# Performance work log

Hardware: AMD Instinct MI355X
Metric: run time of the kernel (lower is better)

## Reference

```python
import jax, jax.numpy as jnp
import numpy as np

B, T, I, H, O = 64, 512, 256, 512, 256

def setup_inputs() -> dict:
    key = jax.random.key(0)
    ks = jax.random.split(key, 12)
    s = 1.0 / np.sqrt(H)
    u = lambda k, shp: jax.random.uniform(k, shp, jnp.float32, -s, s)
    return {
        'x': jax.random.normal(ks[0], (B, T, I), jnp.float32),
        'w_ih0': u(ks[1], (H, I)),  'w_hh0': u(ks[2], (H, H)),
        'b_ih0': u(ks[3], (H,)),    'b_hh0': u(ks[4], (H,)),
        'w_ih1': u(ks[5], (H, H)),  'w_hh1': u(ks[6], (H, H)),
        'b_ih1': u(ks[7], (H,)),    'b_hh1': u(ks[8], (H,)),
        'fc_w': u(ks[9], (O, H)),   'fc_b': u(ks[10], (O,)),
    }

def _rnn_layer(inp, w_ih, w_hh, b_ih, b_hh):
    # inp: [B, T, F] -> precompute input projection once (one big GEMM)
    xp = jnp.einsum('btf,hf->bth', inp, w_ih) + b_ih + b_hh  # [B, T, H]
    def step(h, xt):
        h = jnp.tanh(xt + h @ w_hh.T)  # [B, H]
        return h, h
    h0 = jnp.zeros((inp.shape[0], w_hh.shape[0]), inp.dtype)
    hT, outs = jax.lax.scan(step, h0, jnp.swapaxes(xp, 0, 1))  # outs: [T, B, H]
    return jnp.swapaxes(outs, 0, 1), hT

def reference(x, w_ih0, w_hh0, b_ih0, b_hh0, w_ih1, w_hh1, b_ih1, b_hh1, fc_w, fc_b):
    out0, h0f = _rnn_layer(x, w_ih0, w_hh0, b_ih0, b_hh0)
    out1, h1f = _rnn_layer(out0, w_ih1, w_hh1, b_ih1, b_hh1)
    hidden = jnp.stack([h0f, h1f])                  # [n_layers, B, H]
    out = out1.reshape(-1, out1.shape[-1]) @ fc_w.T + fc_b  # [B*T, O]
    return out, hidden
```

## Files before the change

kernel.cpp:

```cpp
#include <hip/hip_runtime.h>

#define B_  64
#define T_  512
#define I_  256
#define H_  512
#define O_  256
#define JW  2
#define BS  16
#define NG  (B_ / BS)
#define FLAG_STRIDE 32

typedef __attribute__((ext_vector_type(8))) __bf16 bf16x8;
typedef __attribute__((ext_vector_type(4))) float f32x4;

__device__ __forceinline__ unsigned short f2bf(float f) {
    unsigned int u = __float_as_uint(f);
    unsigned int r = (u + 0x7fffu + ((u >> 16) & 1u)) >> 16;
    return (unsigned short)r;
}

__device__ __forceinline__ float tanh_fast(float x) {
    float e = __expf(2.0f * x);
    float d = e + 1.0f;
    float r;
    asm("v_rcp_f32 %0, %1" : "=v"(r) : "v"(d));
    return 1.0f - 2.0f * r;
}

__global__ void cvt_kernel(const float* __restrict__ in, unsigned short* __restrict__ out, int n4) {
    int i = blockIdx.x * blockDim.x + threadIdx.x;
    if (i >= n4) return;
    float4 f = reinterpret_cast<const float4*>(in)[i];
    ushort4 o;
    o.x = f2bf(f.x); o.y = f2bf(f.y); o.z = f2bf(f.z); o.w = f2bf(f.w);
    reinterpret_cast<ushort4*>(out)[i] = o;
}

__global__ __launch_bounds__(256) void gemm_kernel(
    const unsigned short* __restrict__ A,
    const unsigned short* __restrict__ Bw,
    const float* __restrict__ b0,
    const float* __restrict__ b1,
    float* __restrict__ C,
    int M, int N, int K)
{
    const int m0 = blockIdx.x * 64;
    const int n0 = blockIdx.y * 64;
    const int tid = threadIdx.x;
    const int wv = tid >> 6;
    const int l = tid & 63;
    const int lr = l & 15;
    const int lk = (l >> 4) * 8;
    const int arow = m0 + wv * 16 + lr;

    f32x4 acc[4] = {{0,0,0,0},{0,0,0,0},{0,0,0,0},{0,0,0,0}};
    const int nks = K / 32;
    for (int ks = 0; ks < nks; ++ks) {
        bf16x8 a = *reinterpret_cast<const bf16x8*>(A + (size_t)arow * K + ks * 32 + lk);
        #pragma unroll
        for (int nt = 0; nt < 4; ++nt) {
            bf16x8 b = *reinterpret_cast<const bf16x8*>(Bw + (size_t)(n0 + nt * 16 + lr) * K + ks * 32 + lk);
            acc[nt] = __builtin_amdgcn_mfma_f32_16x16x32_bf16(a, b, acc[nt], 0, 0, 0);
        }
    }
    #pragma unroll
    for (int nt = 0; nt < 4; ++nt) {
        #pragma unroll
        for (int r = 0; r < 4; ++r) {
            int row = m0 + wv * 16 + (l >> 4) * 4 + r;
            int col = n0 + nt * 16 + lr;
            float v = acc[nt][r];
            if (b0) v += b0[col];
            if (b1) v += b1[col];
            C[(size_t)row * N + col] = v;
        }
    }
}

#define LDW8(ARR, BASE) \
    asm volatile( \
        "global_load_dwordx4 %0, %8, %9 offset:0\n\t" \
        "global_load_dwordx4 %1, %8, %9 offset:64\n\t" \
        "global_load_dwordx4 %2, %8, %9 offset:128\n\t" \
        "global_load_dwordx4 %3, %8, %9 offset:192\n\t" \
        "global_load_dwordx4 %4, %8, %9 offset:256\n\t" \
        "global_load_dwordx4 %5, %8, %9 offset:320\n\t" \
        "global_load_dwordx4 %6, %8, %9 offset:384\n\t" \
        "global_load_dwordx4 %7, %8, %9 offset:448\n\t" \
        "s_waitcnt vmcnt(0)" \
        : "=&v"(ARR[0]), "=&v"(ARR[1]), "=&v"(ARR[2]), "=&v"(ARR[3]), \
          "=&v"(ARR[4]), "=&v"(ARR[5]), "=&v"(ARR[6]), "=&v"(ARR[7]) \
        : "v"(BASE), "s"(w))

#define STORE_BUNDLE(PK, VHP, VOUT) \
    asm volatile( \
        "global_store_dword %16, %0, %21 sc0 sc1\n\t" \
        "global_store_dword %16, %1, %21 offset:1024 sc0 sc1\n\t" \
        "global_store_dword %16, %2, %21 offset:2048 sc0 sc1\n\t" \
        "global_store_dword %16, %3, %21 offset:3072 sc0 sc1\n\t" \
        "global_store_dword %16, %4, %21 offset:32 sc0 sc1\n\t" \
        "global_store_dword %16, %5, %21 offset:1056 sc0 sc1\n\t" \
        "global_store_dword %16, %6, %21 offset:2080 sc0 sc1\n\t" \
        "global_store_dword %16, %7, %21 offset:3104 sc0 sc1\n\t" \
        "global_store_dword %16, %8, %21 offset:64 sc0 sc1\n\t" \
        "global_store_dword %16, %9, %21 offset:1088 sc0 sc1\n\t" \
        "global_store_dword %16, %10, %21 offset:2112 sc0 sc1\n\t" \
        "global_store_dword %16, %11, %21 offset:3136 sc0 sc1\n\t" \
        "global_store_dword %16, %12, %21 offset:96 sc0 sc1\n\t" \
        "global_store_dword %16, %13, %21 offset:1120 sc0 sc1\n\t" \
        "global_store_dword %16, %14, %21 offset:2144 sc0 sc1\n\t" \
        "global_store_dword %16, %15, %21 offset:3168 sc0 sc1\n\t" \
        "global_store_dword %17, %0, %22\n\t" \
        "global_store_dword %18, %1, %22\n\t" \
        "global_store_dword %19, %2, %22\n\t" \
        "global_store_dword %20, %3, %22\n\t" \
        "global_store_dword %17, %4, %22 offset:32\n\t" \
        "global_store_dword %18, %5, %22 offset:32\n\t" \
        "global_store_dword %19, %6, %22 offset:32\n\t" \
        "global_store_dword %20, %7, %22 offset:32\n\t" \
        "global_store_dword %17, %8, %22 offset:64\n\t" \
        "global_store_dword %18, %9, %22 offset:64\n\t" \
        "global_store_dword %19, %10, %22 offset:64\n\t" \
        "global_store_dword %20, %11, %22 offset:64\n\t" \
        "global_store_dword %17, %12, %22 offset:96\n\t" \
        "global_store_dword %18, %13, %22 offset:96\n\t" \
        "global_store_dword %19, %14, %22 offset:96\n\t" \
        "global_store_dword %20, %15, %22 offset:96\n\t" \
        "s_waitcnt vmcnt(16)" \
        :: "v"(PK[0]), "v"(PK[1]), "v"(PK[2]), "v"(PK[3]), \
           "v"(PK[4]), "v"(PK[5]), "v"(PK[6]), "v"(PK[7]), \
           "v"(PK[8]), "v"(PK[9]), "v"(PK[10]), "v"(PK[11]), \
           "v"(PK[12]), "v"(PK[13]), "v"(PK[14]), "v"(PK[15]), \
           "v"(VHP), "v"(VOUT[0]), "v"(VOUT[1]), "v"(VOUT[2]), "v"(VOUT[3]), \
           "s"(h_buf), "s"(out_bf) \
        : "memory")

__global__ __launch_bounds__(256, 1) void recur_kernel(
    const float* __restrict__ xp,
    const unsigned short* __restrict__ w,
    unsigned short* __restrict__ out_bf,
    float* __restrict__ h_final,
    unsigned short* __restrict__ h_buf,
    int* __restrict__ flags)
{
    __shared__ __align__(16) unsigned short lds[16 * 272];

    const int bid = blockIdx.x;
    const int g   = bid >> 1;
    const int jw  = bid & 1;
    const int pjw = jw ^ 1;
    const int b0  = g * BS;
    const int tid = threadIdx.x;
    const int wv  = tid >> 6;
    const int l   = tid & 63;
    const int lr  = l & 15;
    const int lk  = (l >> 4) * 8;
    const int jn0 = jw * 256 + wv * 64;
    const int arow = b0 + lr;
    const int erow_l = (l >> 4) * 4;
    const int erow_g = b0 + erow_l;

    bf16x8 bwo[4][8], bwp[4][8];
    #pragma unroll
    for (int nt = 0; nt < 4; ++nt) {
        unsigned int vo = (unsigned)((jn0 + nt * 16 + lr) * (H_ * 2) + jw  * 512 + lk * 2);
        unsigned int vp = (unsigned)((jn0 + nt * 16 + lr) * (H_ * 2) + pjw * 512 + lk * 2);
        LDW8(bwo[nt], vo);
        LDW8(bwp[nt], vp);
    }

    unsigned int vxpr[4], vout[4];
    #pragma unroll
    for (int r = 0; r < 4; ++r) {
        vxpr[r] = (unsigned)((((erow_g + r) * T_) * H_ + jn0 + lr) * 4);
        vout[r] = (unsigned)(((erow_g + r) * T_) * H_ * 2 + (jn0 + lr) * 2);
    }
    const unsigned int vaf0p = (unsigned)(arow * (H_ * 2) + pjw * 512 + lk * 2);
    const unsigned int vhs0  = (unsigned)(erow_g * (H_ * 2) + (jn0 + lr) * 2);
    const unsigned int fpeer = (unsigned)((bid ^ 1) * FLAG_STRIDE * 4);
    const unsigned int fself = (unsigned)(bid * FLAG_STRIDE * 4);
    const int cb = wv * 32 + (lr >> 1);

    {
        float xpr[16];
        asm volatile(
            "global_load_dword %0, %16, %20\n\t"
            "global_load_dword %1, %17, %20\n\t"
            "global_load_dword %2, %18, %20\n\t"
            "global_load_dword %3, %19, %20\n\t"
            "global_load_dword %4, %16, %20 offset:64\n\t"
            "global_load_dword %5, %17, %20 offset:64\n\t"
            "global_load_dword %6, %18, %20 offset:64\n\t"
            "global_load_dword %7, %19, %20 offset:64\n\t"
            "global_load_dword %8, %16, %20 offset:128\n\t"
            "global_load_dword %9, %17, %20 offset:128\n\t"
            "global_load_dword %10, %18, %20 offset:128\n\t"
            "global_load_dword %11, %19, %20 offset:128\n\t"
            "global_load_dword %12, %16, %20 offset:192\n\t"
            "global_load_dword %13, %17, %20 offset:192\n\t"
            "global_load_dword %14, %18, %20 offset:192\n\t"
            "global_load_dword %15, %19, %20 offset:192\n\t"
            "s_waitcnt vmcnt(0)"
            : "=&v"(xpr[0]), "=&v"(xpr[1]), "=&v"(xpr[2]), "=&v"(xpr[3]),
              "=&v"(xpr[4]), "=&v"(xpr[5]), "=&v"(xpr[6]), "=&v"(xpr[7]),
              "=&v"(xpr[8]), "=&v"(xpr[9]), "=&v"(xpr[10]), "=&v"(xpr[11]),
              "=&v"(xpr[12]), "=&v"(xpr[13]), "=&v"(xpr[14]), "=&v"(xpr[15])
            : "v"(vxpr[0]), "v"(vxpr[1]), "v"(vxpr[2]), "v"(vxpr[3]), "s"(xp));

        unsigned int pk[16];
        #pragma unroll
        for (int nt = 0; nt < 4; ++nt)
            #pragma unroll
            for (int r = 0; r < 4; ++r) {
                int i = nt * 4 + r;
                float hv = tanh_fast(xpr[i]);
                unsigned int mine = f2bf(hv);
                unsigned int oth = (unsigned int)__shfl_xor((int)mine, 1, 64);
                pk[i] = mine | (oth << 16);
            }
        if (!(lr & 1)) {
            unsigned int* lw = (unsigned int*)lds;
            #pragma unroll
            for (int nt = 0; nt < 4; ++nt)
                #pragma unroll
                for (int r = 0; r < 4; ++r)
                    lw[(erow_l + r) * 136 + cb + nt * 8] = pk[nt * 4 + r];
            unsigned int vh_p = vhs0 + (1u << 16);
            STORE_BUNDLE(pk, vh_p, vout);
        }
        __syncthreads();
        if (tid == 0) {
            int nv = 1;
            asm volatile("global_store_dword %0, %1, %2 sc0 sc1"
                         :: "v"(fself), "v"(nv), "s"(flags) : "memory");
        }
        #pragma unroll
        for (int r = 0; r < 4; ++r) { vxpr[r] += H_ * 4; vout[r] += H_ * 2; }
    }

    for (int t = 1; t < T_; ++t) {
        f32x4 acc[4] = {{0,0,0,0},{0,0,0,0},{0,0,0,0},{0,0,0,0}};
        bf16x8 afo[8];
        const unsigned short* lrb = lds + lr * 272 + lk;
        #pragma unroll
        for (int i = 0; i < 8; ++i)
            afo[i] = *reinterpret_cast<const bf16x8*>(lrb + i * 32);
        #pragma unroll
        for (int i = 0; i < 8; ++i) {
            acc[0] = __builtin_amdgcn_mfma_f32_16x16x32_bf16(afo[i], bwo[0][i], acc[0], 0, 0, 0);
            acc[1] = __builtin_amdgcn_mfma_f32_16x16x32_bf16(afo[i], bwo[1][i], acc[1], 0, 0, 0);
            acc[2] = __builtin_amdgcn_mfma_f32_16x16x32_bf16(afo[i], bwo[2][i], acc[2], 0, 0, 0);
            acc[3] = __builtin_amdgcn_mfma_f32_16x16x32_bf16(afo[i], bwo[3][i], acc[3], 0, 0, 0);
        }
        __builtin_amdgcn_sched_barrier(0);

        if (tid == 0) {
            int fv;
            do {
                asm volatile("global_load_dword %0, %1, %2 sc0 sc1\n\ts_waitcnt vmcnt(0)"
                             : "=v"(fv) : "v"(fpeer), "s"(flags) : "memory");
            } while (fv < t);
        }
        __syncthreads();

        float xpr[16];
        bf16x8 afp[8];
        {
            const unsigned int vafp = vaf0p + ((unsigned)(t & 1) << 16);
            asm volatile(
                "global_load_dword %0, %24, %28\n\t"
                "global_load_dword %1, %25, %28\n\t"
                "global_load_dword %2, %26, %28\n\t"
                "global_load_dword %3, %27, %28\n\t"
                "global_load_dword %4, %24, %28 offset:64\n\t"
                "global_load_dword %5, %25, %28 offset:64\n\t"
                "global_load_dword %6, %26, %28 offset:64\n\t"
                "global_load_dword %7, %27, %28 offset:64\n\t"
                "global_load_dword %8, %24, %28 offset:128\n\t"
                "global_load_dword %9, %25, %28 offset:128\n\t"
                "global_load_dword %10, %26, %28 offset:128\n\t"
                "global_load_dword %11, %27, %28 offset:128\n\t"
                "global_load_dword %12, %24, %28 offset:192\n\t"
                "global_load_dword %13, %25, %28 offset:192\n\t"
                "global_load_dword %14, %26, %28 offset:192\n\t"
                "global_load_dword %15, %27, %28 offset:192\n\t"
                "global_load_dwordx4 %16, %29, %30 sc0 sc1\n\t"
                "global_load_dwordx4 %17, %29, %30 offset:64 sc0 sc1\n\t"
                "global_load_dwordx4 %18, %29, %30 offset:128 sc0 sc1\n\t"
                "global_load_dwordx4 %19, %29, %30 offset:192 sc0 sc1\n\t"
                "global_load_dwordx4 %20, %29, %30 offset:256 sc0 sc1\n\t"
                "global_load_dwordx4 %21, %29, %30 offset:320 sc0 sc1\n\t"
                "global_load_dwordx4 %22, %29, %30 offset:384 sc0 sc1\n\t"
                "global_load_dwordx4 %23, %29, %30 offset:448 sc0 sc1\n\t"
                "s_waitcnt vmcnt(0)"
                : "=&v"(xpr[0]), "=&v"(xpr[1]), "=&v"(xpr[2]), "=&v"(xpr[3]),
                  "=&v"(xpr[4]), "=&v"(xpr[5]), "=&v"(xpr[6]), "=&v"(xpr[7]),
                  "=&v"(xpr[8]), "=&v"(xpr[9]), "=&v"(xpr[10]), "=&v"(xpr[11]),
                  "=&v"(xpr[12]), "=&v"(xpr[13]), "=&v"(xpr[14]), "=&v"(xpr[15]),
                  "=&v"(afp[0]), "=&v"(afp[1]), "=&v"(afp[2]), "=&v"(afp[3]),
                  "=&v"(afp[4]), "=&v"(afp[5]), "=&v"(afp[6]), "=&v"(afp[7])
                : "v"(vxpr[0]), "v"(vxpr[1]), "v"(vxpr[2]), "v"(vxpr[3]),
                  "s"(xp), "v"(vafp), "s"(h_buf));
        }
        __builtin_amdgcn_sched_barrier(0);

        #pragma unroll
        for (int i = 0; i < 8; ++i) {
            acc[0] = __builtin_amdgcn_mfma_f32_16x16x32_bf16(afp[i], bwp[0][i], acc[0], 0, 0, 0);
            acc[1] = __builtin_amdgcn_mfma_f32_16x16x32_bf16(afp[i], bwp[1][i], acc[1], 0, 0, 0);
            acc[2] = __builtin_amdgcn_mfma_f32_16x16x32_bf16(afp[i], bwp[2][i], acc[2], 0, 0, 0);
            acc[3] = __builtin_amdgcn_mfma_f32_16x16x32_bf16(afp[i], bwp[3][i], acc[3], 0, 0, 0);
        }

        unsigned int pk[16];
        #pragma unroll
        for (int nt = 0; nt < 4; ++nt)
            #pragma unroll
            for (int r = 0; r < 4; ++r) {
                int i = nt * 4 + r;
                float pre = acc[nt][r] + xpr[i];
                float hv = tanh_fast(pre);
                if (t == T_ - 1)
                    h_final[(size_t)(erow_g + r) * H_ + jn0 + nt * 16 + lr] = hv;
                unsigned int mine = f2bf(hv);
                unsigned int oth = (unsigned int)__shfl_xor((int)mine, 1, 64);
                pk[i] = mine | (oth << 16);
            }
        if (!(lr & 1)) {
            unsigned int* lw = (unsigned int*)lds;
            #pragma unroll
            for (int nt = 0; nt < 4; ++nt)
                #pragma unroll
                for (int r = 0; r < 4; ++r)
                    lw[(erow_l + r) * 136 + cb + nt * 8] = pk[nt * 4 + r];
            unsigned int vh_p = vhs0 + ((unsigned)((t + 1) & 1) << 16);
            STORE_BUNDLE(pk, vh_p, vout);
        }
        __syncthreads();
        if (tid == 0) {
            int nv = t + 1;
            asm volatile("global_store_dword %0, %1, %2 sc0 sc1"
                         :: "v"(fself), "v"(nv), "s"(flags) : "memory");
        }
        #pragma unroll
        for (int r = 0; r < 4; ++r) { vxpr[r] += H_ * 4; vout[r] += H_ * 2; }
    }
}

#define OFF_XBF    ((size_t)0)
#define OFF_WIH0   ((size_t)16777216)
#define OFF_WHH0   ((size_t)17039360)
#define OFF_WIH1   ((size_t)17563648)
#define OFF_WHH1   ((size_t)18087936)
#define OFF_FCW    ((size_t)18612224)
#define OFF_XP     ((size_t)18874368)
#define OFF_OUTBF  ((size_t)85983232)
#define OFF_HBUF0  ((size_t)119537664)
#define OFF_HBUF1  ((size_t)119668736)
#define OFF_FLAGS  ((size_t)119799808)
#define WS_NEED    ((size_t)119803904)

extern "C" void kernel_launch(void* const* d_in, const int* in_sizes, int n_in,
                              void* d_out, int out_size, void* d_ws, size_t ws_size,
                              hipStream_t stream) {
    if (ws_size < WS_NEED) return;
    const float* x     = (const float*)d_in[0];
    const float* w_ih0 = (const float*)d_in[1];
    const float* w_hh0 = (const float*)d_in[2];
    const float* b_ih0 = (const float*)d_in[3];
    const float* b_hh0 = (const float*)d_in[4];
    const float* w_ih1 = (const float*)d_in[5];
    const float* w_hh1 = (const float*)d_in[6];
    const float* b_ih1 = (const float*)d_in[7];
    const float* b_hh1 = (const float*)d_in[8];
    const float* fc_w  = (const float*)d_in[9];
    const float* fc_b  = (const float*)d_in[10];

    char* ws = (char*)d_ws;
    unsigned short* x_bf     = (unsigned short*)(ws + OFF_XBF);
    unsigned short* w_ih0_bf = (unsigned short*)(ws + OFF_WIH0);
    unsigned short* w_hh0_bf = (unsigned short*)(ws + OFF_WHH0);
    unsigned short* w_ih1_bf = (unsigned short*)(ws + OFF_WIH1);
    unsigned short* w_hh1_bf = (unsigned short*)(ws + OFF_WHH1);
    unsigned short* fc_w_bf  = (unsigned short*)(ws + OFF_FCW);
    float*          xp       = (float*)(ws + OFF_XP);
    unsigned short* out_bf   = (unsigned short*)(ws + OFF_OUTBF);
    unsigned short* h_buf0   = (unsigned short*)(ws + OFF_HBUF0);
    unsigned short* h_buf1   = (unsigned short*)(ws + OFF_HBUF1);
    int*            flags0   = (int*)(ws + OFF_FLAGS);
    int*            flags1   = flags0 + NG * JW * FLAG_STRIDE;

    float* out  = (float*)d_out;
    float* hid0 = out + (size_t)B_ * T_ * O_;
    float* hid1 = hid0 + (size_t)B_ * H_;

    hipMemsetAsync(ws + OFF_HBUF0, 0, 131072 * 2 + 4096, stream);

    auto cvt = [&](const float* in, unsigned short* o, int n) {
        int n4 = n / 4;
        cvt_kernel<<<(n4 + 255) / 256, 256, 0, stream>>>(in, o, n4);
    };
    cvt(x,     x_bf,     B_ * T_ * I_);
    cvt(w_ih0, w_ih0_bf, H_ * I_);
    cvt(w_hh0, w_hh0_bf, H_ * H_);
    cvt(w_ih1, w_ih1_bf, H_ * H_);
    cvt(w_hh1, w_hh1_bf, H_ * H_);
    cvt(fc_w,  fc_w_bf,  O_ * H_);

    const int M = B_ * T_;

    gemm_kernel<<<dim3(M / 64, H_ / 64), 256, 0, stream>>>(
        x_bf, w_ih0_bf, b_ih0, b_hh0, xp, M, H_, I_);

    recur_kernel<<<NG * JW, 256, 0, stream>>>(xp, w_hh0_bf, out_bf, hid0, h_buf0, flags0);

    gemm_kernel<<<dim3(M / 64, H_ / 64), 256, 0, stream>>>(
        out_bf, w_ih1_bf, b_ih1, b_hh1, xp, M, H_, H_);

    recur_kernel<<<NG * JW, 256, 0, stream>>>(xp, w_hh1_bf, out_bf, hid1, h_buf1, flags1);

    gemm_kernel<<<dim3(M / 64, O_ / 64), 256, 0, stream>>>(
        out_bf, fc_w_bf, fc_b, nullptr, out, M, O_, H_);
}
```

Before: 4.439 ms.

## Replace flag-based peer sync with sentinel-tagged data slots in recurrence

The recurrence kernel no longer has a separate flag write plus a thread-0 spin and block barrier before loading the peer block's hidden half. Each block now writes its hidden slice into one of four ring slots pre-filled with a sentinel value, and every lane polls its own slot data until no sentinel remains, then re-poisons the consumed slot. This removes a flag round-trip and one __syncthreads per timestep, and lets the local-half MFMA overlap the wait. The cost is an extra memset between layers and reliance on the sentinel bit pattern never occurring in real bf16 pairs. The LDS row padding is also changed from 272 to 280 halfwords.

```diff
diff --git a/kernel.cpp b/kernel.cpp
--- a/kernel.cpp
+++ b/kernel.cpp
@@ -8,10 +8,13 @@
 #define JW  2
 #define BS  16
 #define NG  (B_ / BS)
-#define FLAG_STRIDE 32
+#define SENT 0x7F7F7F7Fu
+#define SLOT_BYTES 8192
+#define BLK_SLOT_STRIDE 32768
 
 typedef __attribute__((ext_vector_type(8))) __bf16 bf16x8;
 typedef __attribute__((ext_vector_type(4))) float f32x4;
+typedef unsigned int u32x4 __attribute__((ext_vector_type(4)));
 
 __device__ __forceinline__ unsigned short f2bf(float f) {
     unsigned int u = __float_as_uint(f);
@@ -92,24 +95,24 @@
           "=&v"(ARR[4]), "=&v"(ARR[5]), "=&v"(ARR[6]), "=&v"(ARR[7]) \
         : "v"(BASE), "s"(w))
 
-#define STORE_BUNDLE(PK, VHP, VOUT) \
+#define STORE_SLOT_OUT(PK, VSLW, VOUT) \
     asm volatile( \
         "global_store_dword %16, %0, %21 sc0 sc1\n\t" \
-        "global_store_dword %16, %1, %21 offset:1024 sc0 sc1\n\t" \
-        "global_store_dword %16, %2, %21 offset:2048 sc0 sc1\n\t" \
-        "global_store_dword %16, %3, %21 offset:3072 sc0 sc1\n\t" \
+        "global_store_dword %16, %1, %21 offset:512 sc0 sc1\n\t" \
+        "global_store_dword %16, %2, %21 offset:1024 sc0 sc1\n\t" \
+        "global_store_dword %16, %3, %21 offset:1536 sc0 sc1\n\t" \
         "global_store_dword %16, %4, %21 offset:32 sc0 sc1\n\t" \
-        "global_store_dword %16, %5, %21 offset:1056 sc0 sc1\n\t" \
-        "global_store_dword %16, %6, %21 offset:2080 sc0 sc1\n\t" \
-        "global_store_dword %16, %7, %21 offset:3104 sc0 sc1\n\t" \
+        "global_store_dword %16, %5, %21 offset:544 sc0 sc1\n\t" \
+        "global_store_dword %16, %6, %21 offset:1056 sc0 sc1\n\t" \
+        "global_store_dword %16, %7, %21 offset:1568 sc0 sc1\n\t" \
         "global_store_dword %16, %8, %21 offset:64 sc0 sc1\n\t" \
-        "global_store_dword %16, %9, %21 offset:1088 sc0 sc1\n\t" \
-        "global_store_dword %16, %10, %21 offset:2112 sc0 sc1\n\t" \
-        "global_store_dword %16, %11, %21 offset:3136 sc0 sc1\n\t" \
+        "global_store_dword %16, %9, %21 offset:576 sc0 sc1\n\t" \
+        "global_store_dword %16, %10, %21 offset:1088 sc0 sc1\n\t" \
+        "global_store_dword %16, %11, %21 offset:1600 sc0 sc1\n\t" \
         "global_store_dword %16, %12, %21 offset:96 sc0 sc1\n\t" \
-        "global_store_dword %16, %13, %21 offset:1120 sc0 sc1\n\t" \
-        "global_store_dword %16, %14, %21 offset:2144 sc0 sc1\n\t" \
-        "global_store_dword %16, %15, %21 offset:3168 sc0 sc1\n\t" \
+        "global_store_dword %16, %13, %21 offset:608 sc0 sc1\n\t" \
+        "global_store_dword %16, %14, %21 offset:1120 sc0 sc1\n\t" \
+        "global_store_dword %16, %15, %21 offset:1632 sc0 sc1\n\t" \
         "global_store_dword %17, %0, %22\n\t" \
         "global_store_dword %18, %1, %22\n\t" \
         "global_store_dword %19, %2, %22\n\t" \
@@ -125,14 +128,13 @@
         "global_store_dword %17, %12, %22 offset:96\n\t" \
         "global_store_dword %18, %13, %22 offset:96\n\t" \
         "global_store_dword %19, %14, %22 offset:96\n\t" \
-        "global_store_dword %20, %15, %22 offset:96\n\t" \
-        "s_waitcnt vmcnt(16)" \
+        "global_store_dword %20, %15, %22 offset:96" \
         :: "v"(PK[0]), "v"(PK[1]), "v"(PK[2]), "v"(PK[3]), \
            "v"(PK[4]), "v"(PK[5]), "v"(PK[6]), "v"(PK[7]), \
            "v"(PK[8]), "v"(PK[9]), "v"(PK[10]), "v"(PK[11]), \
            "v"(PK[12]), "v"(PK[13]), "v"(PK[14]), "v"(PK[15]), \
-           "v"(VHP), "v"(VOUT[0]), "v"(VOUT[1]), "v"(VOUT[2]), "v"(VOUT[3]), \
-           "s"(h_buf), "s"(out_bf) \
+           "v"(VSLW), "v"(VOUT[0]), "v"(VOUT[1]), "v"(VOUT[2]), "v"(VOUT[3]), \
+           "s"(slots), "s"(out_bf) \
         : "memory")
 
 __global__ __launch_bounds__(256, 1) void recur_kernel(
@@ -140,10 +142,9 @@
     const unsigned short* __restrict__ w,
     unsigned short* __restrict__ out_bf,
     float* __restrict__ h_final,
-    unsigned short* __restrict__ h_buf,
-    int* __restrict__ flags)
+    unsigned short* __restrict__ slots)
 {
-    __shared__ __align__(16) unsigned short lds[16 * 272];
+    __shared__ __align__(16) unsigned short lds[16 * 280];
 
     const int bid = blockIdx.x;
     const int g   = bid >> 1;
@@ -156,7 +157,6 @@
     const int lr  = l & 15;
     const int lk  = (l >> 4) * 8;
     const int jn0 = jw * 256 + wv * 64;
-    const int arow = b0 + lr;
     const int erow_l = (l >> 4) * 4;
     const int erow_g = b0 + erow_l;
 
@@ -175,11 +175,12 @@
         vxpr[r] = (unsigned)((((erow_g + r) * T_) * H_ + jn0 + lr) * 4);
         vout[r] = (unsigned)(((erow_g + r) * T_) * H_ * 2 + (jn0 + lr) * 2);
     }
-    const unsigned int vaf0p = (unsigned)(arow * (H_ * 2) + pjw * 512 + lk * 2);
-    const unsigned int vhs0  = (unsigned)(erow_g * (H_ * 2) + (jn0 + lr) * 2);
-    const unsigned int fpeer = (unsigned)((bid ^ 1) * FLAG_STRIDE * 4);
-    const unsigned int fself = (unsigned)(bid * FLAG_STRIDE * 4);
-    const int cb = wv * 32 + (lr >> 1);
+    const unsigned int slot_wr_b = (unsigned)(bid * BLK_SLOT_STRIDE);
+    const unsigned int slot_rd_b = (unsigned)((bid ^ 1) * BLK_SLOT_STRIDE);
+    const unsigned int vslr_base = slot_rd_b + (unsigned)(lr * 512 + lk * 2);
+    const unsigned int vslw_base = slot_wr_b + (unsigned)(erow_l * 512 + (wv * 64 + lr) * 2);
+    const unsigned int vsent_base = slot_rd_b + (unsigned)(wv * 2048 + l * 16);
+    const u32x4 sentq = {SENT, SENT, SENT, SENT};
 
     {
         float xpr[16];
@@ -220,96 +221,112 @@
             }
         if (!(lr & 1)) {
             unsigned int* lw = (unsigned int*)lds;
+            const int cb = wv * 32 + (lr >> 1);
             #pragma unroll
             for (int nt = 0; nt < 4; ++nt)
                 #pragma unroll
                 for (int r = 0; r < 4; ++r)
-                    lw[(erow_l + r) * 136 + cb + nt * 8] = pk[nt * 4 + r];
-            unsigned int vh_p = vhs0 + (1u << 16);
-            STORE_BUNDLE(pk, vh_p, vout);
+                    lw[(erow_l + r) * 140 + cb + nt * 8] = pk[nt * 4 + r];
+            unsigned int vslw = vslw_base + 1u * SLOT_BYTES;
+            STORE_SLOT_OUT(pk, vslw, vout);
         }
         __syncthreads();
-        if (tid == 0) {
-            int nv = 1;
-            asm volatile("global_store_dword %0, %1, %2 sc0 sc1"
-                         :: "v"(fself), "v"(nv), "s"(flags) : "memory");
-        }
         #pragma unroll
         for (int r = 0; r < 4; ++r) { vxpr[r] += H_ * 4; vout[r] += H_ * 2; }
     }
 
     for (int t = 1; t < T_; ++t) {
         f32x4 acc[4] = {{0,0,0,0},{0,0,0,0},{0,0,0,0},{0,0,0,0}};
-        bf16x8 afo[8];
-        const unsigned short* lrb = lds + lr * 272 + lk;
+        {
+            bf16x8 afo[8];
+            const unsigned short* lrb = lds + lr * 280 + lk;
+            #pragma unroll
+            for (int i = 0; i < 8; ++i)
+                afo[i] = *reinterpret_cast<const bf16x8*>(lrb + i * 32);
+            #pragma unroll
+            for (int i = 0; i < 8; ++i) {
+                acc[0] = __builtin_amdgcn_mfma_f32_16x16x32_bf16(afo[i], bwo[0][i], acc[0], 0, 0, 0);
+                acc[1] = __builtin_amdgcn_mfma_f32_16x16x32_bf16(afo[i], bwo[1][i], acc[1], 0, 0, 0);
+                acc[2] = __builtin_amdgcn_mfma_f32_16x16x32_bf16(afo[i], bwo[2][i], acc[2], 0, 0, 0);
+                acc[3] = __builtin_amdgcn_mfma_f32_16x16x32_bf16(afo[i], bwo[3][i], acc[3], 0, 0, 0);
+            }
+        }
+        __builtin_amdgcn_sched_barrier(0);
+
+        const unsigned int vslr = vslr_base + (unsigned)(t & 3) * SLOT_BYTES;
+        float xpr[16];
+        u32x4 afp[8];
+        asm volatile(
+            "global_load_dword %0, %24, %28\n\t"
+            "global_load_dword %1, %25, %28\n\t"
+            "global_load_dword %2, %26, %28\n\t"
+            "global_load_dword %3, %27, %28\n\t"
+            "global_load_dword %4, %24, %28 offset:64\n\t"
+            "global_load_dword %5, %25, %28 offset:64\n\t"
+            "global_load_dword %6, %26, %28 offset:64\n\t"
+            "global_load_dword %7, %27, %28 offset:64\n\t"
+            "global_load_dword %8, %24, %28 offset:128\n\t"
+            "global_load_dword %9, %25, %28 offset:128\n\t"
+            "global_load_dword %10, %26, %28 offset:128\n\t"
+            "global_load_dword %11, %27, %28 offset:128\n\t"
+            "global_load_dword %12, %24, %28 offset:192\n\t"
+            "global_load_dword %13, %25, %28 offset:192\n\t"
+            "global_load_dword %14, %26, %28 offset:192\n\t"
+            "global_load_dword %15, %27, %28 offset:192\n\t"
+            "global_load_dwordx4 %16, %29, %30 sc0 sc1\n\t"
+            "global_load_dwordx4 %17, %29, %30 offset:64 sc0 sc1\n\t"
+            "global_load_dwordx4 %18, %29, %30 offset:128 sc0 sc1\n\t"
+            "global_load_dwordx4 %19, %29, %30 offset:192 sc0 sc1\n\t"
+            "global_load_dwordx4 %20, %29, %30 offset:256 sc0 sc1\n\t"
+            "global_load_dwordx4 %21, %29, %30 offset:320 sc0 sc1\n\t"
+            "global_load_dwordx4 %22, %29, %30 offset:384 sc0 sc1\n\t"
+            "global_load_dwordx4 %23, %29, %30 offset:448 sc0 sc1\n\t"
+            "s_waitcnt vmcnt(0)"
+            : "=&v"(xpr[0]), "=&v"(xpr[1]), "=&v"(xpr[2]), "=&v"(xpr[3]),
+              "=&v"(xpr[4]), "=&v"(xpr[5]), "=&v"(xpr[6]), "=&v"(xpr[7]),
+              "=&v"(xpr[8]), "=&v"(xpr[9]), "=&v"(xpr[10]), "=&v"(xpr[11]),
+              "=&v"(xpr[12]), "=&v"(xpr[13]), "=&v"(xpr[14]), "=&v"(xpr[15]),
+              "=&v"(afp[0]), "=&v"(afp[1]), "=&v"(afp[2]), "=&v"(afp[3]),
+              "=&v"(afp[4]), "=&v"(afp[5]), "=&v"(afp[6]), "=&v"(afp[7])
+            : "v"(vxpr[0]), "v"(vxpr[1]), "v"(vxpr[2]), "v"(vxpr[3]),
+              "s"(xp), "v"(vslr), "s"(slots));
+
+        int bad = 0;
         #pragma unroll
         for (int i = 0; i < 8; ++i)
-            afo[i] = *reinterpret_cast<const bf16x8*>(lrb + i * 32);
+            #pragma unroll
+            for (int j = 0; j < 4; ++j)
+                bad |= (afp[i][j] == SENT);
+        while (__any(bad)) {
+            asm volatile(
+                "global_load_dwordx4 %0, %8, %9 sc0 sc1\n\t"
+                "global_load_dwordx4 %1, %8, %9 offset:64 sc0 sc1\n\t"
+                "global_load_dwordx4 %2, %8, %9 offset:128 sc0 sc1\n\t"
+                "global_load_dwordx4 %3, %8, %9 offset:192 sc0 sc1\n\t"
+                "global_load_dwordx4 %4, %8, %9 offset:256 sc0 sc1\n\t"
+                "global_load_dwordx4 %5, %8, %9 offset:320 sc0 sc1\n\t"
+                "global_load_dwordx4 %6, %8, %9 offset:384 sc0 sc1\n\t"
+                "global_load_dwordx4 %7, %8, %9 offset:448 sc0 sc1\n\t"
+                "s_waitcnt vmcnt(0)"
+                : "=&v"(afp[0]), "=&v"(afp[1]), "=&v"(afp[2]), "=&v"(afp[3]),
+                  "=&v"(afp[4]), "=&v"(afp[5]), "=&v"(afp[6]), "=&v"(afp[7])
+                : "v"(vslr), "s"(slots));
+            bad = 0;
+            #pragma unroll
+            for (int i = 0; i < 8; ++i)
+                #pragma unroll
+                for (int j = 0; j < 4; ++j)
+                    bad |= (afp[i][j] == SENT);
+        }
+        __builtin_amdgcn_sched_barrier(0);
+
         #pragma unroll
         for (int i = 0; i < 8; ++i) {
-            acc[0] = __builtin_amdgcn_mfma_f32_16x16x32_bf16(afo[i], bwo[0][i], acc[0], 0, 0, 0);
-            acc[1] = __builtin_amdgcn_mfma_f32_16x16x32_bf16(afo[i], bwo[1][i], acc[1], 0, 0, 0);
-            acc[2] = __builtin_amdgcn_mfma_f32_16x16x32_bf16(afo[i], bwo[2][i], acc[2], 0, 0, 0);
-            acc[3] = __builtin_amdgcn_mfma_f32_16x16x32_bf16(afo[i], bwo[3][i], acc[3], 0, 0, 0);
-        }
-        __builtin_amdgcn_sched_barrier(0);
-
-        if (tid == 0) {
-            int fv;
-            do {
-                asm volatile("global_load_dword %0, %1, %2 sc0 sc1\n\ts_waitcnt vmcnt(0)"
-                             : "=v"(fv) : "v"(fpeer), "s"(flags) : "memory");
-            } while (fv < t);
-        }
-        __syncthreads();
-
-        float xpr[16];
-        bf16x8 afp[8];
-        {
-            const unsigned int vafp = vaf0p + ((unsigned)(t & 1) << 16);
-            asm volatile(
-                "global_load_dword %0, %24, %28\n\t"
-                "global_load_dword %1, %25, %28\n\t"
-                "global_load_dword %2, %26, %28\n\t"
-                "global_load_dword %3, %27, %28\n\t"
-                "global_load_dword %4, %24, %28 offset:64\n\t"
-                "global_load_dword %5, %25, %28 offset:64\n\t"
-                "global_load_dword %6, %26, %28 offset:64\n\t"
-                "global_load_dword %7, %27, %28 offset:64\n\t"
-                "global_load_dword %8, %24, %28 offset:128\n\t"
-                "global_load_dword %9, %25, %28 offset:128\n\t"
-                "global_load_dword %10, %26, %28 offset:128\n\t"
-                "global_load_dword %11, %27, %28 offset:128\n\t"
-                "global_load_dword %12, %24, %28 offset:192\n\t"
-                "global_load_dword %13, %25, %28 offset:192\n\t"
-                "global_load_dword %14, %26, %28 offset:192\n\t"
-                "global_load_dword %15, %27, %28 offset:192\n\t"
-                "global_load_dwordx4 %16, %29, %30 sc0 sc1\n\t"
-                "global_load_dwordx4 %17, %29, %30 offset:64 sc0 sc1\n\t"
-                "global_load_dwordx4 %18, %29, %30 offset:128 sc0 sc1\n\t"
-                "global_load_dwordx4 %19, %29, %30 offset:192 sc0 sc1\n\t"
-                "global_load_dwordx4 %20, %29, %30 offset:256 sc0 sc1\n\t"
-                "global_load_dwordx4 %21, %29, %30 offset:320 sc0 sc1\n\t"
-                "global_load_dwordx4 %22, %29, %30 offset:384 sc0 sc1\n\t"
-                "global_load_dwordx4 %23, %29, %30 offset:448 sc0 sc1\n\t"
-                "s_waitcnt vmcnt(0)"
-                : "=&v"(xpr[0]), "=&v"(xpr[1]), "=&v"(xpr[2]), "=&v"(xpr[3]),
-                  "=&v"(xpr[4]), "=&v"(xpr[5]), "=&v"(xpr[6]), "=&v"(xpr[7]),
-                  "=&v"(xpr[8]), "=&v"(xpr[9]), "=&v"(xpr[10]), "=&v"(xpr[11]),
-                  "=&v"(xpr[12]), "=&v"(xpr[13]), "=&v"(xpr[14]), "=&v"(xpr[15]),
-                  "=&v"(afp[0]), "=&v"(afp[1]), "=&v"(afp[2]), "=&v"(afp[3]),
-                  "=&v"(afp[4]), "=&v"(afp[5]), "=&v"(afp[6]), "=&v"(afp[7])
-                : "v"(vxpr[0]), "v"(vxpr[1]), "v"(vxpr[2]), "v"(vxpr[3]),
-                  "s"(xp), "v"(vafp), "s"(h_buf));
-        }
-        __builtin_amdgcn_sched_barrier(0);
-
-        #pragma unroll
-        for (int i = 0; i < 8; ++i) {
-            acc[0] = __builtin_amdgcn_mfma_f32_16x16x32_bf16(afp[i], bwp[0][i], acc[0], 0, 0, 0);
-            acc[1] = __builtin_amdgcn_mfma_f32_16x16x32_bf16(afp[i], bwp[1][i], acc[1], 0, 0, 0);
-            acc[2] = __builtin_amdgcn_mfma_f32_16x16x32_bf16(afp[i], bwp[2][i], acc[2], 0, 0, 0);
-            acc[3] = __builtin_amdgcn_mfma_f32_16x16x32_bf16(afp[i], bwp[3][i], acc[3], 0, 0, 0);
+            bf16x8 a = __builtin_bit_cast(bf16x8, afp[i]);
+            acc[0] = __builtin_amdgcn_mfma_f32_16x16x32_bf16(a, bwp[0][i], acc[0], 0, 0, 0);
+            acc[1] = __builtin_amdgcn_mfma_f32_16x16x32_bf16(a, bwp[1][i], acc[1], 0, 0, 0);
+            acc[2] = __builtin_amdgcn_mfma_f32_16x16x32_bf16(a, bwp[2][i], acc[2], 0, 0, 0);
+            acc[3] = __builtin_amdgcn_mfma_f32_16x16x32_bf16(a, bwp[3][i], acc[3], 0, 0, 0);
         }
 
         unsigned int pk[16];
@@ -328,19 +345,24 @@
             }
         if (!(lr & 1)) {
             unsigned int* lw = (unsigned int*)lds;
+            const int cb = wv * 32 + (lr >> 1);
             #pragma unroll
             for (int nt = 0; nt < 4; ++nt)
                 #pragma unroll
                 for (int r = 0; r < 4; ++r)
-                    lw[(erow_l + r) * 136 + cb + nt * 8] = pk[nt * 4 + r];
-            unsigned int vh_p = vhs0 + ((unsigned)((t + 1) & 1) << 16);
-            STORE_BUNDLE(pk, vh_p, vout);
-        }
+                    lw[(erow_l + r) * 140 + cb + nt * 8] = pk[nt * 4 + r];
+            unsigned int vslw = vslw_base + (unsigned)((t + 1) & 3) * SLOT_BYTES;
+            STORE_SLOT_OUT(pk, vslw, vout);
+        }
+
         __syncthreads();
-        if (tid == 0) {
-            int nv = t + 1;
-            asm volatile("global_store_dword %0, %1, %2 sc0 sc1"
-                         :: "v"(fself), "v"(nv), "s"(flags) : "memory");
+
+        {
+            unsigned int vs = vsent_base + (unsigned)(t & 3) * SLOT_BYTES;
+            asm volatile(
+                "global_store_dwordx4 %0, %1, %2 sc0 sc1\n\t"
+                "global_store_dwordx4 %0, %1, %2 offset:1024 sc0 sc1"
+                :: "v"(vs), "v"(sentq), "s"(slots) : "memory");
         }
         #pragma unroll
         for (int r = 0; r < 4; ++r) { vxpr[r] += H_ * 4; vout[r] += H_ * 2; }
@@ -355,10 +377,8 @@
 #define OFF_FCW    ((size_t)18612224)
 #define OFF_XP     ((size_t)18874368)
 #define OFF_OUTBF  ((size_t)85983232)
-#define OFF_HBUF0  ((size_t)119537664)
-#define OFF_HBUF1  ((size_t)119668736)
-#define OFF_FLAGS  ((size_t)119799808)
-#define WS_NEED    ((size_t)119803904)
+#define OFF_SLOTS  ((size_t)119537664)
+#define WS_NEED    ((size_t)119799808)
 
 extern "C" void kernel_launch(void* const* d_in, const int* in_sizes, int n_in,
                               void* d_out, int out_size, void* d_ws, size_t ws_size,
@@ -385,16 +405,13 @@
     unsigned short* fc_w_bf  = (unsigned short*)(ws + OFF_FCW);
     float*          xp       = (float*)(ws + OFF_XP);
     unsigned short* out_bf   = (unsigned short*)(ws + OFF_OUTBF);
-    unsigned short* h_buf0   = (unsigned short*)(ws + OFF_HBUF0);
-    unsigned short* h_buf1   = (unsigned short*)(ws + OFF_HBUF1);
-    int*            flags0   = (int*)(ws + OFF_FLAGS);
-    int*            flags1   = flags0 + NG * JW * FLAG_STRIDE;
+    unsigned short* slots    = (unsigned short*)(ws + OFF_SLOTS);
 
     float* out  = (float*)d_out;
     float* hid0 = out + (size_t)B_ * T_ * O_;
     float* hid1 = hid0 + (size_t)B_ * H_;
 
-    hipMemsetAsync(ws + OFF_HBUF0, 0, 131072 * 2 + 4096, stream);
+    hipMemsetAsync(ws + OFF_SLOTS, 0x7F, 262144, stream);
 
     auto cvt = [&](const float* in, unsigned short* o, int n) {
         int n4 = n / 4;
@@ -412,12 +429,14 @@
     gemm_kernel<<<dim3(M / 64, H_ / 64), 256, 0, stream>>>(
         x_bf, w_ih0_bf, b_ih0, b_hh0, xp, M, H_, I_);
 
-    recur_kernel<<<NG * JW, 256, 0, stream>>>(xp, w_hh0_bf, out_bf, hid0, h_buf0, flags0);
+    recur_kernel<<<NG * JW, 256, 0, stream>>>(xp, w_hh0_bf, out_bf, hid0, slots);
 
     gemm_kernel<<<dim3(M / 64, H_ / 64), 256, 0, stream>>>(
         out_bf, w_ih1_bf, b_ih1, b_hh1, xp, M, H_, H_);
 
-    recur_kernel<<<NG * JW, 256, 0, stream>>>(xp, w_hh1_bf, out_bf, hid1, h_buf1, flags1);
+    hipMemsetAsync(ws + OFF_SLOTS, 0x7F, 262144, stream);
+
+    recur_kernel<<<NG * JW, 256, 0, stream>>>(xp, w_hh1_bf, out_bf, hid1, slots);
 
     gemm_kernel<<<dim3(M / 64, O_ / 64), 256, 0, stream>>>(
         out_bf, fc_w_bf, fc_b, nullptr, out, M, O_, H_);
```

After: 3.599 ms. 18.9% less time.
